# Optimization experiments

Hardware: AMD Instinct MI355X
Metric: run time of the kernel (lower is better)

The kernel has to match this reference:

```python
import jax, jax.numpy as jnp
import numpy as np

N_NODES = 100000
N_EDGES = 1600000
IN_DIM = 256
OUT_DIM = 128
SELF_LOOP_W = 2.0  # improved=True


def setup_inputs() -> dict:
    key = jax.random.key(0)
    ks = jax.random.split(key, 9)
    x = jax.random.normal(ks[0], (N_NODES, IN_DIM), dtype=jnp.float32)
    edge_index = jax.random.randint(ks[1], (2, N_EDGES), 0, N_NODES, dtype=jnp.int64)
    edge_weight = jax.random.uniform(ks[2], (N_EDGES,), dtype=jnp.float32)
    s1 = 1.0 / np.sqrt(IN_DIM)
    s2 = 1.0 / np.sqrt(OUT_DIM)
    W1 = jax.random.normal(ks[3], (IN_DIM, OUT_DIM), dtype=jnp.float32) * s1
    b1 = jnp.zeros((OUT_DIM,), dtype=jnp.float32)
    W_mu = jax.random.normal(ks[4], (OUT_DIM, OUT_DIM), dtype=jnp.float32) * s2
    b_mu = jnp.zeros((OUT_DIM,), dtype=jnp.float32)
    W_var = jax.random.normal(ks[5], (OUT_DIM, OUT_DIM), dtype=jnp.float32) * s2
    b_var = jnp.zeros((OUT_DIM,), dtype=jnp.float32)
    return {"x": x, "edge_index": edge_index, "edge_weight": edge_weight,
            "W1": W1, "b1": b1, "W_mu": W_mu, "b_mu": b_mu,
            "W_var": W_var, "b_var": b_var}


def _gcn_norm(edge_index, edge_weight, num_nodes):
    # add self loops with fill value 2.0 (improved=True), then symmetric norm
    loop = jnp.arange(num_nodes, dtype=edge_index.dtype)
    row = jnp.concatenate([edge_index[0], loop])
    col = jnp.concatenate([edge_index[1], loop])
    ew = jnp.concatenate([edge_weight,
                          jnp.full((num_nodes,), SELF_LOOP_W, dtype=edge_weight.dtype)])
    deg = jax.ops.segment_sum(ew, col, num_segments=num_nodes)
    dis = jnp.where(deg > 0, jax.lax.rsqrt(jnp.where(deg > 0, deg, 1.0)), 0.0)
    norm = dis[row] * ew * dis[col]
    return row, col, norm


def _gcn_conv(x, row, col, norm, W, b, num_nodes):
    xw = x @ W                      # [N, out]
    msg = xw[row] * norm[:, None]   # [E+N, out] per-edge messages
    out = jax.ops.segment_sum(msg, col, num_segments=num_nodes)
    return out + b


def reference(x, edge_index, edge_weight, W1, b1, W_mu, b_mu, W_var, b_var):
    n = x.shape[0]
    row, col, norm = _gcn_norm(edge_index, edge_weight, n)
    feat = jax.nn.relu(_gcn_conv(x, row, col, norm, W1, b1, n))
    mu = _gcn_conv(feat, row, col, norm, W_mu, b_mu, n)
    var = _gcn_conv(feat, row, col, norm, W_var, b_var, n)
    return (mu, var)
```

## Files before the change

kernel.cpp:

```cpp
#include <hip/hip_runtime.h>
#include <hip/hip_bf16.h>

#define CDIV(a,b) (((a)+(b)-1)/(b))

typedef __attribute__((ext_vector_type(8))) short short8;
typedef __attribute__((ext_vector_type(4))) float f32x4;

static __device__ inline short f2bf(float f) {
    union { __hip_bfloat16 h; short s; } u;
    u.h = __float2bfloat16(f);
    return u.s;
}
static __device__ inline ushort f2bfu(float f) { return (ushort)f2bf(f); }
static __device__ inline float bfu_lo(uint v) { return __uint_as_float(v << 16); }
static __device__ inline float bfu_hi(uint v) { return __uint_as_float(v & 0xffff0000u); }


__global__ __launch_bounds__(512) void k_init(const float* __restrict__ W1,
                                              short* __restrict__ W1t,
                                              const float* __restrict__ Wmu,
                                              const float* __restrict__ Wvar,
                                              short* __restrict__ Wcat) {
    int i = blockIdx.x * 512 + threadIdx.x;
    if (i < 128 * 256) {
        int k = i % 256, col = i / 256;
        W1t[i] = f2bf(W1[(size_t)k * 128 + col]);
    } else if (i < 2 * 128 * 256) {
        int j = i - 128 * 256;
        int k = j & 127, col = j >> 7;
        float v = (col < 128) ? Wmu[(size_t)k * 128 + col] : Wvar[(size_t)k * 128 + (col - 128)];
        Wcat[j] = f2bf(v);
    }
}


__global__ __launch_bounds__(512) void k_bhist(const int* __restrict__ coli,
                                               int* __restrict__ bhist,
                                               int E, int chunk, int nbk) {
    __shared__ int h[256];
    int b = blockIdx.x, t = threadIdx.x, nblk = gridDim.x;
    for (int i = t; i < nbk; i += 512) h[i] = 0;
    __syncthreads();
    int e0 = b * chunk, e1 = min(E, e0 + chunk);
    for (int e = e0 + t; e < e1; e += 512)
        atomicAdd(&h[coli[e] >> 9], 1);
    __syncthreads();
    for (int i = t; i < nbk; i += 512)
        bhist[i * nblk + b] = h[i];
}

__global__ __launch_bounds__(256) void kscanA(const int* __restrict__ in,
                                              int* __restrict__ out,
                                              int* __restrict__ part, int n) {
    int t = threadIdx.x;
    int base = blockIdx.x * 1024 + t * 4;
    int v0 = (base + 0 < n) ? in[base + 0] : 0;
    int v1 = (base + 1 < n) ? in[base + 1] : 0;
    int v2 = (base + 2 < n) ? in[base + 2] : 0;
    int v3 = (base + 3 < n) ? in[base + 3] : 0;
    int tsum = v0 + v1 + v2 + v3;
    int lane = t & 63, wv = t >> 6;
    int val = tsum;
    #pragma unroll
    for (int d = 1; d < 64; d <<= 1) {
        int u = __shfl_up(val, d, 64);
        if (lane >= d) val += u;
    }
    __shared__ int ws[4];
    if (lane == 63) ws[wv] = val;
    __syncthreads();
    int woff = 0;
    #pragma unroll
    for (int i = 0; i < 4; ++i) if (i < wv) woff += ws[i];
    int excl = woff + val - tsum;
    if (base + 0 < n) out[base + 0] = excl;  excl += v0;
    if (base + 1 < n) out[base + 1] = excl;  excl += v1;
    if (base + 2 < n) out[base + 2] = excl;  excl += v2;
    if (base + 3 < n) out[base + 3] = excl;
    if (t == 255) part[blockIdx.x] = woff + val;
}

__global__ __launch_bounds__(128) void kscanB(int* part, int nb) {
    int t = threadIdx.x;
    int v = (t < nb) ? part[t] : 0;
    int lane = t & 63, wv = t >> 6;
    int val = v;
    #pragma unroll
    for (int d = 1; d < 64; d <<= 1) {
        int u = __shfl_up(val, d, 64);
        if (lane >= d) val += u;
    }
    __shared__ int ws[2];
    if (lane == 63) ws[wv] = val;
    __syncthreads();
    int woff = (wv == 1) ? ws[0] : 0;
    if (t < nb) part[t] = woff + val - v;
}

__global__ __launch_bounds__(256) void kscanC(int* __restrict__ out,
                                              const int* __restrict__ part, int n) {
    int i = blockIdx.x * 256 + threadIdx.x;
    if (i < n) out[i] += part[i >> 10];
}

__global__ __launch_bounds__(512) void k_bucket(const int* __restrict__ rowi,
                                                const int* __restrict__ coli,
                                                const float* __restrict__ ew,
                                                const int* __restrict__ excl,
                                                int* __restrict__ bx,
                                                int* __restrict__ bw,
                                                int E, int chunk, int nbk) {
    __shared__ int cur[256];
    int b = blockIdx.x, t = threadIdx.x, nblk = gridDim.x;
    for (int i = t; i < nbk; i += 512) cur[i] = 0;
    __syncthreads();
    int e0 = b * chunk, e1 = min(E, e0 + chunk);
    for (int e = e0 + t; e < e1; e += 512) {
        int c = coli[e];
        int bk = c >> 9;
        int pos = excl[bk * nblk + b] + atomicAdd(&cur[bk], 1);
        bx[pos] = ((c & 511) << 17) | rowi[e];
        bw[pos] = __float_as_int(ew[e]);
    }
}

__global__ __launch_bounds__(512) void k_fine2(const int* __restrict__ bx,
                                               const int* __restrict__ bw,
                                               const int* __restrict__ excl,
                                               int* __restrict__ row_ptr,
                                               float* __restrict__ dis,
                                               int E, int nblk, int n) {
    __shared__ int cnt[512], ews[512];
    int bk = blockIdx.x, t = threadIdx.x;
    cnt[t] = 0; ews[t] = 0;
    __syncthreads();
    int s0 = excl[bk * nblk];
    int s1 = (bk + 1 < gridDim.x) ? excl[(bk + 1) * nblk] : E;
    for (int p = s0 + t; p < s1; p += 512) {
        int cl = bx[p] >> 17;
        atomicAdd(&cnt[cl], 1);
        int q = (int)(__int_as_float(bw[p]) * 16777216.0f + 0.5f);
        atomicAdd(&ews[cl], q);
    }
    __syncthreads();
    int v = cnt[t];
    int lane = t & 63, wv = t >> 6;
    int val = v;
    #pragma unroll
    for (int d = 1; d < 64; d <<= 1) {
        int u = __shfl_up(val, d, 64);
        if (lane >= d) val += u;
    }
    __shared__ int ws2[8];
    if (lane == 63) ws2[wv] = val;
    __syncthreads();
    int woff = 0;
    #pragma unroll
    for (int i = 0; i < 8; ++i) if (i < wv) woff += ws2[i];
    int lexcl = woff + val - v;
    int c = bk * 512 + t;
    if (c < n) {
        row_ptr[c] = s0 + lexcl;
        dis[c] = rsqrtf(2.0f + (float)ews[t] * (1.0f / 16777216.0f));
    }
    if (bk == 0 && t == 0) row_ptr[n] = E;
}

__global__ __launch_bounds__(512) void k_place(const int* __restrict__ bx,
                                               const int* __restrict__ bw,
                                               const int* __restrict__ excl,
                                               const int* __restrict__ row_ptr,
                                               const float* __restrict__ dis,
                                               int2* __restrict__ csr,
                                               int E, int nblk, int n) {
    __shared__ int cur[512];
    int bk = blockIdx.x, t = threadIdx.x;
    cur[t] = 0;
    __syncthreads();
    int s0 = excl[bk * nblk];
    int s1 = (bk + 1 < gridDim.x) ? excl[(bk + 1) * nblk] : E;
    int cbase = bk * 512;
    for (int p = s0 + t; p < s1; p += 512) {
        int u = bx[p];
        int cl = u >> 17, r = u & 0x1FFFF;
        int pos = row_ptr[cbase + cl] + atomicAdd(&cur[cl], 1);
        csr[pos] = make_int2(r, __float_as_int(dis[r] * __int_as_float(bw[p])));
    }
}


__global__ __launch_bounds__(512) void k_gemm1(const float* __restrict__ A,
                                               const short* __restrict__ Bt,
                                               ushort* __restrict__ C, int n) {
    const int K = 256, KH = 128;
    __shared__ short Blds[128 * KH];
    int t = threadIdx.x;

    int wave = t >> 6, lane = t & 63;
    int lg = lane >> 4, lr = lane & 15;
    long row_base = (long)blockIdx.x * 256 + wave * 32;

    long ra0 = row_base + lr;      if (ra0 > n - 1) ra0 = n - 1;
    long ra1 = row_base + 16 + lr; if (ra1 > n - 1) ra1 = n - 1;

    f32x4 acc[2][8];
    #pragma unroll
    for (int i = 0; i < 2; ++i)
        #pragma unroll
        for (int j = 0; j < 8; ++j) acc[i][j] = (f32x4){0.f, 0.f, 0.f, 0.f};

    const float* pa0 = A + ra0 * K + lg * 8;
    const float* pa1 = A + ra1 * K + lg * 8;

    #pragma unroll
    for (int p = 0; p < 2; ++p) {
        if (p) __syncthreads();
        const int CHK = KH / 8;
        for (int c = t; c < 128 * CHK; c += 512) {
            int colw = c / CHK;
            int kb  = (c % CHK) * 16;
            int dst = colw * (KH * 2) + (kb ^ ((colw & 7) << 4));
            *(float4*)((char*)Blds + dst) =
                *(const float4*)((const char*)Bt + (size_t)colw * (K * 2) + p * (KH * 2) + kb);
        }
        __syncthreads();

        for (int k0 = 0; k0 < KH; k0 += 32) {
            int kg = p * KH + k0;
            float4 x0 = *(const float4*)(pa0 + kg);
            float4 x1 = *(const float4*)(pa0 + kg + 4);
            float4 y0 = *(const float4*)(pa1 + kg);
            float4 y1 = *(const float4*)(pa1 + kg + 4);
            short8 a0, a1;
            a0[0]=f2bf(x0.x); a0[1]=f2bf(x0.y); a0[2]=f2bf(x0.z); a0[3]=f2bf(x0.w);
            a0[4]=f2bf(x1.x); a0[5]=f2bf(x1.y); a0[6]=f2bf(x1.z); a0[7]=f2bf(x1.w);
            a1[0]=f2bf(y0.x); a1[1]=f2bf(y0.y); a1[2]=f2bf(y0.z); a1[3]=f2bf(y0.w);
            a1[4]=f2bf(y1.x); a1[5]=f2bf(y1.y); a1[6]=f2bf(y1.z); a1[7]=f2bf(y1.w);

            int kb = (k0 + lg * 8) * 2;
            #pragma unroll
            for (int cb = 0; cb < 8; ++cb) {
                int colm = cb * 16 + lr;
                short8 bfr = *(short8*)((char*)Blds + colm * (KH * 2) + (kb ^ ((colm & 7) << 4)));
                acc[0][cb] = __builtin_amdgcn_mfma_f32_16x16x32_bf16(a0, bfr, acc[0][cb], 0, 0, 0);
                acc[1][cb] = __builtin_amdgcn_mfma_f32_16x16x32_bf16(a1, bfr, acc[1][cb], 0, 0, 0);
            }
        }
    }

    #pragma unroll
    for (int rf = 0; rf < 2; ++rf) {
        #pragma unroll
        for (int cb = 0; cb < 8; ++cb) {
            int colm = cb * 16 + lr;
            #pragma unroll
            for (int r = 0; r < 4; ++r) {
                long row = row_base + rf * 16 + lg * 4 + r;
                if (row < n) C[row * 128 + colm] = f2bfu(acc[rf][cb][r]);
            }
        }
    }
}


template<int OUTMODE>
__global__ __launch_bounds__(256) void k_agg(const uint2* __restrict__ src,
                                             const int* __restrict__ row_ptr,
                                             const int2* __restrict__ csr,
                                             const float* __restrict__ dis,
                                             const float* __restrict__ bias,
                                             uint2* __restrict__ dst, int n) {
    int wid = (blockIdx.x * 256 + threadIdx.x) >> 6;
    int lane = threadIdx.x & 63;
    int hb = lane >> 5, lc = lane & 31;
    if (wid >= n) return;
    int e0 = row_ptr[wid], e1 = row_ptr[wid + 1];

    float p00=0.f,p01=0.f,p02=0.f,p03=0.f;
    float p10=0.f,p11=0.f,p12=0.f,p13=0.f;
    float p20=0.f,p21=0.f,p22=0.f,p23=0.f;
    float p30=0.f,p31=0.f,p32=0.f,p33=0.f;

    int e = e0;
    for (; e + 15 < e1; e += 16) {
        int2 c0 = csr[e      + hb], c1 = csr[e + 2  + hb];
        int2 c2 = csr[e + 4  + hb], c3 = csr[e + 6  + hb];
        int2 c4 = csr[e + 8  + hb], c5 = csr[e + 10 + hb];
        int2 c6 = csr[e + 12 + hb], c7 = csr[e + 14 + hb];
        uint2 v0 = src[(size_t)c0.x * 32 + lc];
        uint2 v1 = src[(size_t)c1.x * 32 + lc];
        uint2 v2 = src[(size_t)c2.x * 32 + lc];
        uint2 v3 = src[(size_t)c3.x * 32 + lc];
        uint2 v4 = src[(size_t)c4.x * 32 + lc];
        uint2 v5 = src[(size_t)c5.x * 32 + lc];
        uint2 v6 = src[(size_t)c6.x * 32 + lc];
        uint2 v7 = src[(size_t)c7.x * 32 + lc];
        float w0 = __int_as_float(c0.y), w1 = __int_as_float(c1.y);
        float w2 = __int_as_float(c2.y), w3 = __int_as_float(c3.y);
        float w4 = __int_as_float(c4.y), w5 = __int_as_float(c5.y);
        float w6 = __int_as_float(c6.y), w7 = __int_as_float(c7.y);
        p00 += w0 * bfu_lo(v0.x); p01 += w0 * bfu_hi(v0.x);
        p02 += w0 * bfu_lo(v0.y); p03 += w0 * bfu_hi(v0.y);
        p10 += w1 * bfu_lo(v1.x); p11 += w1 * bfu_hi(v1.x);
        p12 += w1 * bfu_lo(v1.y); p13 += w1 * bfu_hi(v1.y);
        p20 += w2 * bfu_lo(v2.x); p21 += w2 * bfu_hi(v2.x);
        p22 += w2 * bfu_lo(v2.y); p23 += w2 * bfu_hi(v2.y);
        p30 += w3 * bfu_lo(v3.x); p31 += w3 * bfu_hi(v3.x);
        p32 += w3 * bfu_lo(v3.y); p33 += w3 * bfu_hi(v3.y);
        p00 += w4 * bfu_lo(v4.x); p01 += w4 * bfu_hi(v4.x);
        p02 += w4 * bfu_lo(v4.y); p03 += w4 * bfu_hi(v4.y);
        p10 += w5 * bfu_lo(v5.x); p11 += w5 * bfu_hi(v5.x);
        p12 += w5 * bfu_lo(v5.y); p13 += w5 * bfu_hi(v5.y);
        p20 += w6 * bfu_lo(v6.x); p21 += w6 * bfu_hi(v6.x);
        p22 += w6 * bfu_lo(v6.y); p23 += w6 * bfu_hi(v6.y);
        p30 += w7 * bfu_lo(v7.x); p31 += w7 * bfu_hi(v7.x);
        p32 += w7 * bfu_lo(v7.y); p33 += w7 * bfu_hi(v7.y);
    }
    for (; e + 7 < e1; e += 8) {
        int2 c0 = csr[e + hb],     c1 = csr[e + 2 + hb];
        int2 c2 = csr[e + 4 + hb], c3 = csr[e + 6 + hb];
        uint2 v0 = src[(size_t)c0.x * 32 + lc];
        uint2 v1 = src[(size_t)c1.x * 32 + lc];
        uint2 v2 = src[(size_t)c2.x * 32 + lc];
        uint2 v3 = src[(size_t)c3.x * 32 + lc];
        float w0 = __int_as_float(c0.y), w1 = __int_as_float(c1.y);
        float w2 = __int_as_float(c2.y), w3 = __int_as_float(c3.y);
        p00 += w0 * bfu_lo(v0.x); p01 += w0 * bfu_hi(v0.x);
        p02 += w0 * bfu_lo(v0.y); p03 += w0 * bfu_hi(v0.y);
        p10 += w1 * bfu_lo(v1.x); p11 += w1 * bfu_hi(v1.x);
        p12 += w1 * bfu_lo(v1.y); p13 += w1 * bfu_hi(v1.y);
        p20 += w2 * bfu_lo(v2.x); p21 += w2 * bfu_hi(v2.x);
        p22 += w2 * bfu_lo(v2.y); p23 += w2 * bfu_hi(v2.y);
        p30 += w3 * bfu_lo(v3.x); p31 += w3 * bfu_hi(v3.x);
        p32 += w3 * bfu_lo(v3.y); p33 += w3 * bfu_hi(v3.y);
    }
    for (; e + 1 < e1; e += 2) {
        int2 c = csr[e + hb];
        uint2 v = src[(size_t)c.x * 32 + lc];
        float w = __int_as_float(c.y);
        p00 += w * bfu_lo(v.x); p01 += w * bfu_hi(v.x);
        p02 += w * bfu_lo(v.y); p03 += w * bfu_hi(v.y);
    }
    if (e < e1 && hb == 0) {
        int2 c = csr[e];
        uint2 v = src[(size_t)c.x * 32 + lc];
        float w = __int_as_float(c.y);
        p10 += w * bfu_lo(v.x); p11 += w * bfu_hi(v.x);
        p12 += w * bfu_lo(v.y); p13 += w * bfu_hi(v.y);
    }

    float x0 = (p00 + p10) + (p20 + p30);
    float x1 = (p01 + p11) + (p21 + p31);
    float x2 = (p02 + p12) + (p22 + p32);
    float x3 = (p03 + p13) + (p23 + p33);
    x0 = x0 + __shfl_xor(x0, 32);
    x1 = x1 + __shfl_xor(x1, 32);
    x2 = x2 + __shfl_xor(x2, 32);
    x3 = x3 + __shfl_xor(x3, 32);

    float dc = dis[wid];
    uint2 sv = src[(size_t)wid * 32 + lc];
    float sw = 2.f * dc * dc;
    float o0 = dc * x0 + sw * bfu_lo(sv.x);
    float o1 = dc * x1 + sw * bfu_hi(sv.x);
    float o2 = dc * x2 + sw * bfu_lo(sv.y);
    float o3 = dc * x3 + sw * bfu_hi(sv.y);
    if constexpr (OUTMODE == 0) {
        float4 bv = *(const float4*)(bias + lc * 4);
        o0 += bv.x; o1 += bv.y; o2 += bv.z; o3 += bv.w;
        o0 = fmaxf(o0, 0.f); o1 = fmaxf(o1, 0.f);
        o2 = fmaxf(o2, 0.f); o3 = fmaxf(o3, 0.f);
    }
    if (hb == 0)
        dst[(size_t)wid * 32 + lc] =
            make_uint2((uint)f2bfu(o0) | ((uint)f2bfu(o1) << 16),
                       (uint)f2bfu(o2) | ((uint)f2bfu(o3) << 16));
}


__global__ __launch_bounds__(512) void k_gemm2(const short* __restrict__ A,
                                               const short* __restrict__ Bt,
                                               const float* __restrict__ bmu,
                                               const float* __restrict__ bvar,
                                               float* __restrict__ out,
                                               int n) {
    const int K = 128;
    __shared__ short Blds[256 * K];
    int t = threadIdx.x;

    const int CHK = K / 8;
    for (int c = t; c < 256 * CHK; c += 512) {
        int col = c / CHK;
        int kb  = (c % CHK) * 16;
        int dst = col * (K * 2) + (kb ^ ((col & 7) << 4));
        *(float4*)((char*)Blds + dst) =
            *(const float4*)((const char*)Bt + (size_t)col * (K * 2) + kb);
    }
    __syncthreads();

    int wave = t >> 6, lane = t & 63;
    int lg = lane >> 4, lr = lane & 15;
    int colbase = (wave & 1) * 128;
    long row_base = (long)blockIdx.x * 128 + (wave >> 1) * 32;

    long ra0 = row_base + lr;      if (ra0 > n - 1) ra0 = n - 1;
    long ra1 = row_base + 16 + lr; if (ra1 > n - 1) ra1 = n - 1;

    f32x4 acc[2][8];
    #pragma unroll
    for (int i = 0; i < 2; ++i)
        #pragma unroll
        for (int j = 0; j < 8; ++j) acc[i][j] = (f32x4){0.f, 0.f, 0.f, 0.f};

    const short* pa0 = A + ra0 * K + lg * 8;
    const short* pa1 = A + ra1 * K + lg * 8;

    #pragma unroll
    for (int k0 = 0; k0 < K; k0 += 32) {
        short8 a0 = *(const short8*)(pa0 + k0);
        short8 a1 = *(const short8*)(pa1 + k0);
        int kb = (k0 + lg * 8) * 2;
        #pragma unroll
        for (int cb = 0; cb < 8; ++cb) {
            int col = colbase + cb * 16 + lr;
            short8 b = *(short8*)((char*)Blds + col * (K * 2) + (kb ^ ((col & 7) << 4)));
            acc[0][cb] = __builtin_amdgcn_mfma_f32_16x16x32_bf16(a0, b, acc[0][cb], 0, 0, 0);
            acc[1][cb] = __builtin_amdgcn_mfma_f32_16x16x32_bf16(a1, b, acc[1][cb], 0, 0, 0);
        }
    }

    #pragma unroll
    for (int rf = 0; rf < 2; ++rf) {
        #pragma unroll
        for (int cb = 0; cb < 8; ++cb) {
            int colc = colbase + cb * 16 + lr;
            bool is_var = colc >= 128;
            int col = is_var ? colc - 128 : colc;
            float bv = is_var ? bvar[col] : bmu[col];
            size_t obase = is_var ? (size_t)n * 128 : 0;
            #pragma unroll
            for (int r = 0; r < 4; ++r) {
                long row = row_base + rf * 16 + lg * 4 + r;
                if (row < n)
                    __builtin_nontemporal_store(acc[rf][cb][r] + bv,
                                                &out[obase + (size_t)row * 128 + col]);
            }
        }
    }
}


extern "C" void kernel_launch(void* const* d_in, const int* in_sizes, int n_in,
                              void* d_out, int out_size, void* d_ws, size_t ws_size,
                              hipStream_t stream) {
    const float* x    = (const float*)d_in[0];
    const int*   ei   = (const int*)d_in[1];
    const float* ew   = (const float*)d_in[2];
    const float* W1   = (const float*)d_in[3];
    const float* b1   = (const float*)d_in[4];
    const float* Wmu  = (const float*)d_in[5];
    const float* bmu  = (const float*)d_in[6];
    const float* Wvar = (const float*)d_in[7];
    const float* bvar = (const float*)d_in[8];

    const int E = in_sizes[2];
    const int N = in_sizes[0] / 256;
    const int* rowi = ei;
    const int* coli = ei + E;

    char* base = (char*)d_ws;
    size_t off = 0;
    auto alloc = [&](size_t bytes) -> void* {
        void* p = base + off;
        off = (off + bytes + 511) & ~(size_t)511;
        return p;
    };
    const int NBLK = 256;
    const int nbk  = CDIV(N, 512);
    const int chunk = CDIV(E, NBLK);
    const int nh   = nbk * NBLK;

    int*   bhist   = (int*)  alloc((size_t)nh * 4);
    int*   excl    = (int*)  alloc((size_t)nh * 4);
    int*   part    = (int*)  alloc(256 * 4);
    int*   bx      = (int*)  alloc((size_t)E * 4);
    int*   bw      = (int*)  alloc((size_t)E * 4);
    int*   row_ptr = (int*)  alloc((size_t)(N + 1) * 4);
    float* dis     = (float*)alloc((size_t)N * 4);
    int2*  csr     = (int2*) alloc((size_t)E * 8);
    uint*  xw      = (uint*) alloc((size_t)N * 64 * 4);
    uint*  feat    = (uint*) alloc((size_t)N * 64 * 4);
    short* W1t     = (short*)alloc((size_t)256 * 128 * 2);
    short* Wcat    = (short*)alloc((size_t)256 * 128 * 2);
    uint*  g       = xw;

    k_init<<<CDIV(2 * 128 * 256, 512), 512, 0, stream>>>(W1, W1t, Wmu, Wvar, Wcat);
    k_gemm1<<<CDIV(N, 256), 512, 0, stream>>>(x, W1t, (ushort*)xw, N);

    k_bhist<<<NBLK, 512, 0, stream>>>(coli, bhist, E, chunk, nbk);
    kscanA<<<CDIV(nh, 1024), 256, 0, stream>>>(bhist, excl, part, nh);
    kscanB<<<1, 128, 0, stream>>>(part, CDIV(nh, 1024));
    kscanC<<<CDIV(nh, 256), 256, 0, stream>>>(excl, part, nh);
    k_bucket<<<NBLK, 512, 0, stream>>>(rowi, coli, ew, excl, bx, bw, E, chunk, nbk);
    k_fine2<<<nbk, 512, 0, stream>>>(bx, bw, excl, row_ptr, dis, E, NBLK, N);
    k_place<<<nbk, 512, 0, stream>>>(bx, bw, excl, row_ptr, dis, csr, E, NBLK, N);

    k_agg<0><<<CDIV(N * 64, 256), 256, 0, stream>>>((const uint2*)xw, row_ptr, csr, dis, b1, (uint2*)feat, N);
    k_agg<1><<<CDIV(N * 64, 256), 256, 0, stream>>>((const uint2*)feat, row_ptr, csr, dis, nullptr, (uint2*)g, N);
    k_gemm2<<<CDIV(N, 128), 512, 0, stream>>>((const short*)g, Wcat, bmu, bvar, (float*)d_out, N);
}
```

Before: 290.4 us.

## Interleave bucket row/weight arrays, shrink agg blocks, drop 16-edge unroll

```diff
diff --git a/kernel.cpp b/kernel.cpp
--- a/kernel.cpp
+++ b/kernel.cpp
@@ -107,8 +107,7 @@
                                                 const int* __restrict__ coli,
                                                 const float* __restrict__ ew,
                                                 const int* __restrict__ excl,
-                                                int* __restrict__ bx,
-                                                int* __restrict__ bw,
+                                                int2* __restrict__ bxw,
                                                 int E, int chunk, int nbk) {
     __shared__ int cur[256];
     int b = blockIdx.x, t = threadIdx.x, nblk = gridDim.x;
@@ -119,13 +118,11 @@
         int c = coli[e];
         int bk = c >> 9;
         int pos = excl[bk * nblk + b] + atomicAdd(&cur[bk], 1);
-        bx[pos] = ((c & 511) << 17) | rowi[e];
-        bw[pos] = __float_as_int(ew[e]);
-    }
-}
-
-__global__ __launch_bounds__(512) void k_fine2(const int* __restrict__ bx,
-                                               const int* __restrict__ bw,
+        bxw[pos] = make_int2(((c & 511) << 17) | rowi[e], __float_as_int(ew[e]));
+    }
+}
+
+__global__ __launch_bounds__(512) void k_fine2(const int2* __restrict__ bxw,
                                                const int* __restrict__ excl,
                                                int* __restrict__ row_ptr,
                                                float* __restrict__ dis,
@@ -137,9 +134,10 @@
     int s0 = excl[bk * nblk];
     int s1 = (bk + 1 < gridDim.x) ? excl[(bk + 1) * nblk] : E;
     for (int p = s0 + t; p < s1; p += 512) {
-        int cl = bx[p] >> 17;
+        int2 u = bxw[p];
+        int cl = u.x >> 17;
         atomicAdd(&cnt[cl], 1);
-        int q = (int)(__int_as_float(bw[p]) * 16777216.0f + 0.5f);
+        int q = (int)(__int_as_float(u.y) * 16777216.0f + 0.5f);
         atomicAdd(&ews[cl], q);
     }
     __syncthreads();
@@ -166,8 +164,7 @@
     if (bk == 0 && t == 0) row_ptr[n] = E;
 }
 
-__global__ __launch_bounds__(512) void k_place(const int* __restrict__ bx,
-                                               const int* __restrict__ bw,
+__global__ __launch_bounds__(512) void k_place(const int2* __restrict__ bxw,
                                                const int* __restrict__ excl,
                                                const int* __restrict__ row_ptr,
                                                const float* __restrict__ dis,
@@ -181,10 +178,10 @@
     int s1 = (bk + 1 < gridDim.x) ? excl[(bk + 1) * nblk] : E;
     int cbase = bk * 512;
     for (int p = s0 + t; p < s1; p += 512) {
-        int u = bx[p];
-        int cl = u >> 17, r = u & 0x1FFFF;
+        int2 u = bxw[p];
+        int cl = u.x >> 17, r = u.x & 0x1FFFF;
         int pos = row_ptr[cbase + cl] + atomicAdd(&cur[cl], 1);
-        csr[pos] = make_int2(r, __float_as_int(dis[r] * __int_as_float(bw[p])));
+        csr[pos] = make_int2(r, __float_as_int(dis[r] * __int_as_float(u.y)));
     }
 }
 
@@ -264,13 +261,13 @@
 
 
 template<int OUTMODE>
-__global__ __launch_bounds__(256) void k_agg(const uint2* __restrict__ src,
+__global__ __launch_bounds__(128) void k_agg(const uint2* __restrict__ src,
                                              const int* __restrict__ row_ptr,
                                              const int2* __restrict__ csr,
                                              const float* __restrict__ dis,
                                              const float* __restrict__ bias,
                                              uint2* __restrict__ dst, int n) {
-    int wid = (blockIdx.x * 256 + threadIdx.x) >> 6;
+    int wid = (blockIdx.x * 128 + threadIdx.x) >> 6;
     int lane = threadIdx.x & 63;
     int hb = lane >> 5, lc = lane & 31;
     if (wid >= n) return;
@@ -282,43 +279,11 @@
     float p30=0.f,p31=0.f,p32=0.f,p33=0.f;
 
     int e = e0;
-    for (; e + 15 < e1; e += 16) {
-        int2 c0 = csr[e      + hb], c1 = csr[e + 2  + hb];
-        int2 c2 = csr[e + 4  + hb], c3 = csr[e + 6  + hb];
-        int2 c4 = csr[e + 8  + hb], c5 = csr[e + 10 + hb];
-        int2 c6 = csr[e + 12 + hb], c7 = csr[e + 14 + hb];
-        uint2 v0 = src[(size_t)c0.x * 32 + lc];
-        uint2 v1 = src[(size_t)c1.x * 32 + lc];
-        uint2 v2 = src[(size_t)c2.x * 32 + lc];
-        uint2 v3 = src[(size_t)c3.x * 32 + lc];
-        uint2 v4 = src[(size_t)c4.x * 32 + lc];
-        uint2 v5 = src[(size_t)c5.x * 32 + lc];
-        uint2 v6 = src[(size_t)c6.x * 32 + lc];
-        uint2 v7 = src[(size_t)c7.x * 32 + lc];
-        float w0 = __int_as_float(c0.y), w1 = __int_as_float(c1.y);
-        float w2 = __int_as_float(c2.y), w3 = __int_as_float(c3.y);
-        float w4 = __int_as_float(c4.y), w5 = __int_as_float(c5.y);
-        float w6 = __int_as_float(c6.y), w7 = __int_as_float(c7.y);
-        p00 += w0 * bfu_lo(v0.x); p01 += w0 * bfu_hi(v0.x);
-        p02 += w0 * bfu_lo(v0.y); p03 += w0 * bfu_hi(v0.y);
-        p10 += w1 * bfu_lo(v1.x); p11 += w1 * bfu_hi(v1.x);
-        p12 += w1 * bfu_lo(v1.y); p13 += w1 * bfu_hi(v1.y);
-        p20 += w2 * bfu_lo(v2.x); p21 += w2 * bfu_hi(v2.x);
-        p22 += w2 * bfu_lo(v2.y); p23 += w2 * bfu_hi(v2.y);
-        p30 += w3 * bfu_lo(v3.x); p31 += w3 * bfu_hi(v3.x);
-        p32 += w3 * bfu_lo(v3.y); p33 += w3 * bfu_hi(v3.y);
-        p00 += w4 * bfu_lo(v4.x); p01 += w4 * bfu_hi(v4.x);
-        p02 += w4 * bfu_lo(v4.y); p03 += w4 * bfu_hi(v4.y);
-        p10 += w5 * bfu_lo(v5.x); p11 += w5 * bfu_hi(v5.x);
-        p12 += w5 * bfu_lo(v5.y); p13 += w5 * bfu_hi(v5.y);
-        p20 += w6 * bfu_lo(v6.x); p21 += w6 * bfu_hi(v6.x);
-        p22 += w6 * bfu_lo(v6.y); p23 += w6 * bfu_hi(v6.y);
-        p30 += w7 * bfu_lo(v7.x); p31 += w7 * bfu_hi(v7.x);
-        p32 += w7 * bfu_lo(v7.y); p33 += w7 * bfu_hi(v7.y);
-    }
     for (; e + 7 < e1; e += 8) {
-        int2 c0 = csr[e + hb],     c1 = csr[e + 2 + hb];
-        int2 c2 = csr[e + 4 + hb], c3 = csr[e + 6 + hb];
+        int2 c0 = csr[e     + hb];
+        int2 c1 = csr[e + 2 + hb];
+        int2 c2 = csr[e + 4 + hb];
+        int2 c3 = csr[e + 6 + hb];
         uint2 v0 = src[(size_t)c0.x * 32 + lc];
         uint2 v1 = src[(size_t)c1.x * 32 + lc];
         uint2 v2 = src[(size_t)c2.x * 32 + lc];
@@ -483,8 +448,7 @@
     int*   bhist   = (int*)  alloc((size_t)nh * 4);
     int*   excl    = (int*)  alloc((size_t)nh * 4);
     int*   part    = (int*)  alloc(256 * 4);
-    int*   bx      = (int*)  alloc((size_t)E * 4);
-    int*   bw      = (int*)  alloc((size_t)E * 4);
+    int2*  bxw     = (int2*) alloc((size_t)E * 8);
     int*   row_ptr = (int*)  alloc((size_t)(N + 1) * 4);
     float* dis     = (float*)alloc((size_t)N * 4);
     int2*  csr     = (int2*) alloc((size_t)E * 8);
@@ -501,11 +465,11 @@
     kscanA<<<CDIV(nh, 1024), 256, 0, stream>>>(bhist, excl, part, nh);
     kscanB<<<1, 128, 0, stream>>>(part, CDIV(nh, 1024));
     kscanC<<<CDIV(nh, 256), 256, 0, stream>>>(excl, part, nh);
-    k_bucket<<<NBLK, 512, 0, stream>>>(rowi, coli, ew, excl, bx, bw, E, chunk, nbk);
-    k_fine2<<<nbk, 512, 0, stream>>>(bx, bw, excl, row_ptr, dis, E, NBLK, N);
-    k_place<<<nbk, 512, 0, stream>>>(bx, bw, excl, row_ptr, dis, csr, E, NBLK, N);
-
-    k_agg<0><<<CDIV(N * 64, 256), 256, 0, stream>>>((const uint2*)xw, row_ptr, csr, dis, b1, (uint2*)feat, N);
-    k_agg<1><<<CDIV(N * 64, 256), 256, 0, stream>>>((const uint2*)feat, row_ptr, csr, dis, nullptr, (uint2*)g, N);
+    k_bucket<<<NBLK, 512, 0, stream>>>(rowi, coli, ew, excl, bxw, E, chunk, nbk);
+    k_fine2<<<nbk, 512, 0, stream>>>(bxw, excl, row_ptr, dis, E, NBLK, N);
+    k_place<<<nbk, 512, 0, stream>>>(bxw, excl, row_ptr, dis, csr, E, NBLK, N);
+
+    k_agg<0><<<CDIV(N * 64, 128), 128, 0, stream>>>((const uint2*)xw, row_ptr, csr, dis, b1, (uint2*)feat, N);
+    k_agg<1><<<CDIV(N * 64, 128), 128, 0, stream>>>((const uint2*)feat, row_ptr, csr, dis, nullptr, (uint2*)g, N);
     k_gemm2<<<CDIV(N, 128), 512, 0, stream>>>((const short*)g, Wcat, bmu, bvar, (float*)d_out, N);
 }
```

Measured after the change: 264.1 us. 1.1x faster.
